# Kernel optimization log

Hardware: AMD Instinct MI355X
Metric: run time of the kernel (lower is better)

## Reference

```python
import jax, jax.numpy as jnp
import numpy as np

N = 50000      # num vertices
M = 10000      # num hyperedges
NNZ = 1600000  # incidence list length (avg degree 32)
D = 128        # in_features == out_features


def setup_inputs() -> dict:
    key = jax.random.key(0)
    k0, k1, k2, k3, k4, k5 = jax.random.split(key, 6)
    X = jax.random.normal(k0, (N, D), dtype=jnp.float32)
    X0 = jax.random.normal(k1, (N, D), dtype=jnp.float32)
    vertex = jax.random.randint(k2, (NNZ,), 0, N)
    edges = jax.random.randint(k3, (NNZ,), 0, M)
    # nn.Linear(D, D, bias=False) weight, kaiming-uniform-ish scale
    W = jax.random.uniform(k4, (D, D), dtype=jnp.float32,
                           minval=-1.0, maxval=1.0) / np.float32(np.sqrt(D))
    alpha = jax.random.uniform(k5, (), dtype=jnp.float32)
    beta = jnp.float32(0.5)
    return {"X": X, "X0": X0, "W": W, "alpha": alpha, "beta": beta,
            "vertex": vertex, "edges": edges}


def _scatter_mean(vals, idx, num_segments):
    # segment mean; empty segments -> 0 (matches torch_scatter 'mean')
    s = jax.ops.segment_sum(vals, idx, num_segments=num_segments)
    cnt = jax.ops.segment_sum(jnp.ones(idx.shape, vals.dtype), idx,
                              num_segments=num_segments)
    return s / jnp.maximum(cnt, 1.0)[:, None]


def reference(X, X0, W, alpha, beta, vertex, edges):
    Xve = X[vertex]                          # [NNZ, D] gather vertex -> incidence
    Xe = _scatter_mean(Xve, edges, M)        # [M, D]   hyperedge features
    Xev = Xe[edges]                          # [NNZ, D] gather edge -> incidence
    Xv = _scatter_mean(Xev, vertex, N)       # [N, D]   back to vertices
    Xi = (1.0 - alpha) * Xv + alpha * X0     # initial-residual mix
    return (1.0 - beta) * Xi + beta * (Xi @ W.T)  # identity-map mix + linear
```

## Files before the change

### kernel.cpp

```cpp
#include <hip/hip_runtime.h>
#include <hip/hip_bf16.h>


#define DD 128
#define NV 50000
#define ME 10000

#define CHUNK 4096
#define NEB 157
#define NVB 196
#define PB_CAP 12288

typedef __hip_bfloat16 bf16;
typedef __attribute__((ext_vector_type(8))) short short8v;
typedef __attribute__((ext_vector_type(4))) float float4v;
typedef __attribute__((ext_vector_type(4))) unsigned uint4v;

#define OFF_XE    0
#define OFF_ELIST 2560000
#define OFF_VLIST 8960000
#define OFF_EPAIR 15360000
#define OFF_VPAIR 21760000
#define OFF_XB    15360000
#define OFF_VOFF  28160000
#define OFF_EOFF  28360064
#define OFF_CBH   28400128
#define OFF_GBE   28401664
#define OFF_GBV   28402304
#define OFF_GCE   28403136
#define OFF_GCV   28403776
#define OFF_FLAG  28404608
#define OFF_WF    28404624
#define WS_USED   28470160

__device__ __forceinline__ float bf2f(unsigned short s) {
    union { unsigned u; float f; } x; x.u = ((unsigned)s) << 16; return x.f;
}
__device__ __forceinline__ unsigned f2bfu(float x) {
    union { bf16 h; unsigned short u; } c; c.h = __float2bfloat16(x); return (unsigned)c.u;
}
__device__ __forceinline__ float loadf(const void* p, long long i, unsigned f32) {
    if (f32) return ((const float*)p)[i];
    return bf2f(((const unsigned short*)p)[i]);
}
__device__ __forceinline__ float u2f_lo(unsigned x) {
    union { unsigned u; float f; } c; c.u = x << 16; return c.f;
}
__device__ __forceinline__ float u2f_hi(unsigned x) {
    union { unsigned u; float f; } c; c.u = x & 0xFFFF0000u; return c.f;
}
__device__ __forceinline__ void acc8(const uint4& u, float* a) {
    a[0] += u2f_lo(u.x); a[1] += u2f_hi(u.x);
    a[2] += u2f_lo(u.y); a[3] += u2f_hi(u.y);
    a[4] += u2f_lo(u.z); a[5] += u2f_hi(u.z);
    a[6] += u2f_lo(u.w); a[7] += u2f_hi(u.w);
}

__device__ __forceinline__ unsigned wave_is_fp32(const unsigned short* p) {
    int l = threadIdx.x & 63;
    int big = 0;
    for (int i = l; i < 256; i += 64) {
        unsigned e = (p[i] >> 7) & 0xFFu;
        if (e >= 0x90u) big++;
    }
    for (int s = 32; s > 0; s >>= 1) big += __shfl_down(big, s);
    return (__shfl(big, 0) >= 4) ? 1u : 0u;
}

__global__ __launch_bounds__(256) void prep_all(const void* X, const void* X0, const void* W,
                                                const void* beta_p,
                                                const int* __restrict__ vertex,
                                                const int* __restrict__ edges,
                                                unsigned* __restrict__ flags,
                                                unsigned short* __restrict__ Wfrag,
                                                unsigned* __restrict__ cbh, int nnz) {
    __shared__ unsigned h[NEB + NVB];
    int b = blockIdx.x, t = threadIdx.x;

    if (b == 0) {
        if (t < 64) {
            const unsigned short* px[3] = {(const unsigned short*)X,
                                           (const unsigned short*)X0,
                                           (const unsigned short*)W};
            for (int k = 0; k < 3; k++) {
                int big = 0;
                for (int i = t; i < 256; i += 64) {
                    unsigned e = (px[k][i] >> 7) & 0xFFu;
                    if (e >= 0x90u) big++;
                }
                for (int s = 32; s > 0; s >>= 1) big += __shfl_down(big, s);
                if (t == 0) flags[k] = (big >= 4) ? 1u : 0u;
            }
            if (t == 0) {
                unsigned short bb = *(const unsigned short*)beta_p;
                flags[3] = (bb == 0x3F00u) ? 0u : 1u;
            }
        }
        return;
    }

    if (b <= 8) {
        int blob = (b - 1) * 256 + t;
        unsigned fW = wave_is_fp32((const unsigned short*)W);
        unsigned short bu = *(const unsigned short*)beta_p;
        unsigned fS = (bu == 0x3F00u) ? 0u : 1u;
        int lane = blob & 63, kk = (blob >> 6) & 3, ct = blob >> 8;
        int nn = lane & 15, quad = lane >> 4;
        int c = ct * 16 + nn;
        int kbase = kk * 32 + quad * 8;
        float beta = loadf(beta_p, 0, fS);
        float omb = 1.f - beta;
        unsigned short hi[8], lo[8];
#pragma unroll
        for (int j = 0; j < 8; j++) {
            float wv = loadf(W, (long long)c * DD + kbase + j, fW);
            float v = beta * wv + ((kbase + j) == c ? omb : 0.f);
            unsigned short hh = (unsigned short)f2bfu(v);
            hi[j] = hh;
            lo[j] = (unsigned short)f2bfu(v - bf2f(hh));
        }
        uint4 ph, pl;
        ph.x = (unsigned)hi[0] | ((unsigned)hi[1] << 16);
        ph.y = (unsigned)hi[2] | ((unsigned)hi[3] << 16);
        ph.z = (unsigned)hi[4] | ((unsigned)hi[5] << 16);
        ph.w = (unsigned)hi[6] | ((unsigned)hi[7] << 16);
        pl.x = (unsigned)lo[0] | ((unsigned)lo[1] << 16);
        pl.y = (unsigned)lo[2] | ((unsigned)lo[3] << 16);
        pl.z = (unsigned)lo[4] | ((unsigned)lo[5] << 16);
        pl.w = (unsigned)lo[6] | ((unsigned)lo[7] << 16);
        ((uint4*)Wfrag)[blob] = ph;
        ((uint4*)Wfrag)[2048 + blob] = pl;
        return;
    }

    int hb = b - 9;
    for (int i = t; i < NEB + NVB; i += 256) h[i] = 0;
    __syncthreads();
    int stride = 512 * 256;
    for (int i = hb * 256 + t; i < nnz; i += stride) {
        atomicAdd(&h[edges[i] >> 6], 1u);
        atomicAdd(&h[NEB + (vertex[i] >> 8)], 1u);
    }
    __syncthreads();
    for (int i = t; i < NEB + NVB; i += 256) {
        unsigned v = h[i];
        if (v) atomicAdd(&cbh[i], v);
    }
}

__global__ __launch_bounds__(256) void conv_x(const void* __restrict__ X,
                                              unsigned short* __restrict__ Xb,
                                              const unsigned* __restrict__ flags) {
    if (!flags[0]) return;
    int i = blockIdx.x * 256 + threadIdx.x;
    if (i >= NV * DD / 8) return;
    const float4* p = (const float4*)X + (size_t)i * 2;
    float4 a = p[0], b = p[1];
    uint4 o;
    o.x = f2bfu(a.x) | (f2bfu(a.y) << 16);
    o.y = f2bfu(a.z) | (f2bfu(a.w) << 16);
    o.z = f2bfu(b.x) | (f2bfu(b.y) << 16);
    o.w = f2bfu(b.z) | (f2bfu(b.w) << 16);
    ((uint4*)Xb)[i] = o;
}

__global__ void scan353(const unsigned* __restrict__ cbh,
                        unsigned* __restrict__ gbe, unsigned* __restrict__ gbv,
                        unsigned* __restrict__ gce, unsigned* __restrict__ gcv,
                        unsigned* __restrict__ voff, unsigned* __restrict__ eoff,
                        int nnz) {
    __shared__ unsigned s[512];
    int t = threadIdx.x;
    unsigned v = (t < NEB + NVB) ? cbh[t] : 0u;
    s[t] = v;
    __syncthreads();
    for (int st = 1; st < 512; st <<= 1) {
        unsigned u = (t >= st) ? s[t - st] : 0u;
        __syncthreads();
        s[t] += u;
        __syncthreads();
    }
    unsigned excl = s[t] - v;
    if (t < NEB) {
        gbe[t] = excl; gce[t] = excl;
    } else if (t < NEB + NVB) {
        unsigned base = s[NEB - 1];
        gbv[t - NEB] = excl - base;
        gcv[t - NEB] = excl - base;
    }
    if (t == 0) {
        gbe[NEB] = (unsigned)nnz;
        gbv[NVB] = (unsigned)nnz;
        eoff[ME] = (unsigned)nnz;
        voff[NV] = (unsigned)nnz;
    }
}

__global__ __launch_bounds__(256) void build_pairs(const int* __restrict__ vertex,
                                                   const int* __restrict__ edges,
                                                   unsigned* __restrict__ gcur_e,
                                                   unsigned* __restrict__ gcur_v,
                                                   unsigned* __restrict__ epairs,
                                                   unsigned* __restrict__ vpairs, int nnz) {
    __shared__ unsigned buf[CHUNK];
    __shared__ unsigned hist[256], scn[256], loff[256], cur[256], gbase[256];
    int t = threadIdx.x;
    int base = blockIdx.x * CHUNK;
    int len = min(CHUNK, nnz - base);
    if (len <= 0) return;

    unsigned pkr[16];

    hist[t] = 0;
    __syncthreads();
#pragma unroll
    for (int it = 0; it < 16; it++) {
        int i = t + it * 256;
        if (i < len) {
            unsigned e = (unsigned)edges[base + i];
            unsigned v = (unsigned)vertex[base + i];
            unsigned pk = (e << 16) | v;
            pkr[it] = pk;
            atomicAdd(&hist[pk >> 22], 1u);
        }
    }
    __syncthreads();
    unsigned hv = hist[t];
    scn[t] = hv;
    __syncthreads();
    for (int st = 1; st < 256; st <<= 1) {
        unsigned u = (t >= st) ? scn[t - st] : 0u;
        __syncthreads();
        scn[t] += u;
        __syncthreads();
    }
    loff[t] = scn[t] - hv;
    cur[t] = scn[t] - hv;
    if (t < NEB && hv > 0) gbase[t] = atomicAdd(&gcur_e[t], hv);
    __syncthreads();
#pragma unroll
    for (int it = 0; it < 16; it++) {
        int i = t + it * 256;
        if (i < len) {
            unsigned pk = pkr[it];
            unsigned p = atomicAdd(&cur[pk >> 22], 1u);
            buf[p] = pk;
        }
    }
    __syncthreads();
    for (int i = t; i < len; i += 256) {
        unsigned pk = buf[i];
        unsigned b = pk >> 22;
        epairs[gbase[b] + (i - loff[b])] = pk;
    }

    __syncthreads();
    hist[t] = 0;
    __syncthreads();
#pragma unroll
    for (int it = 0; it < 16; it++) {
        int i = t + it * 256;
        if (i < len) {
            unsigned pk = buf[i];
            unsigned npk = (pk << 16) | (pk >> 16);
            pkr[it] = npk;
            atomicAdd(&hist[npk >> 24], 1u);
        }
    }
    __syncthreads();
    hv = hist[t];
    scn[t] = hv;
    __syncthreads();
    for (int st = 1; st < 256; st <<= 1) {
        unsigned u = (t >= st) ? scn[t - st] : 0u;
        __syncthreads();
        scn[t] += u;
        __syncthreads();
    }
    loff[t] = scn[t] - hv;
    cur[t] = scn[t] - hv;
    if (t < NVB && hv > 0) gbase[t] = atomicAdd(&gcur_v[t], hv);
    __syncthreads();
#pragma unroll
    for (int it = 0; it < 16; it++) {
        int i = t + it * 256;
        if (i < len) {
            unsigned npk = pkr[it];
            unsigned p = atomicAdd(&cur[npk >> 24], 1u);
            buf[p] = npk;
        }
    }
    __syncthreads();
    for (int i = t; i < len; i += 256) {
        unsigned npk = buf[i];
        unsigned b = npk >> 24;
        vpairs[gbase[b] + (i - loff[b])] = npk;
    }
}

__global__ __launch_bounds__(256) void build_lists(const unsigned* __restrict__ epairs,
                                                   const unsigned* __restrict__ vpairs,
                                                   const unsigned* __restrict__ gbe,
                                                   const unsigned* __restrict__ gbv,
                                                   unsigned* __restrict__ eoff,
                                                   unsigned* __restrict__ voff,
                                                   unsigned short* __restrict__ elist,
                                                   unsigned short* __restrict__ vlist) {
    __shared__ unsigned buf[PB_CAP];
    __shared__ unsigned offs[256], curs[256];
    int b = blockIdx.x, t = threadIdx.x;
    const unsigned* pairs;
    unsigned* off;
    unsigned short* list;
    unsigned s0, s1;
    int k0, nk;
    if (b < NEB) {
        pairs = epairs; off = eoff; list = elist;
        k0 = b << 6; nk = min(64, ME - k0);
        s0 = gbe[b]; s1 = gbe[b + 1];
    } else {
        int bb = b - NEB;
        pairs = vpairs; off = voff; list = vlist;
        k0 = bb << 8; nk = min(256, NV - k0);
        s0 = gbv[bb]; s1 = gbv[bb + 1];
    }
    int len = (int)(s1 - s0);

    curs[t] = 0;
    __syncthreads();
    for (int i = t; i < len; i += 256) {
        unsigned pk = pairs[s0 + i];
        atomicAdd(&curs[(pk >> 16) - k0], 1u);
    }
    __syncthreads();
    unsigned hv = curs[t];
    offs[t] = hv;
    __syncthreads();
    for (int st = 1; st < 256; st <<= 1) {
        unsigned u = (t >= st) ? offs[t - st] : 0u;
        __syncthreads();
        offs[t] += u;
        __syncthreads();
    }
    unsigned my_excl = offs[t] - hv;
    __syncthreads();
    offs[t] = my_excl;
    curs[t] = 0;
    if (t < nk) off[k0 + t] = s0 + my_excl;
    __syncthreads();

    if (len <= PB_CAP) {
        for (int i = t; i < len; i += 256) {
            unsigned pk = pairs[s0 + i];
            int lk = (int)(pk >> 16) - k0;
            unsigned p = offs[lk] + atomicAdd(&curs[lk], 1u);
            buf[p] = pk & 0xFFFFu;
        }
        __syncthreads();
        for (int i = t; i < len; i += 256) list[s0 + i] = (unsigned short)buf[i];
    } else {
        for (int i = t; i < len; i += 256) {
            unsigned pk = pairs[s0 + i];
            int lk = (int)(pk >> 16) - k0;
            unsigned p = offs[lk] + atomicAdd(&curs[lk], 1u);
            list[s0 + p] = (unsigned short)(pk & 0xFFFFu);
        }
    }
}

__global__ __launch_bounds__(256, 8) void edge_agg(const void* __restrict__ X,
                                                   const unsigned short* __restrict__ Xb,
                                                   const unsigned* __restrict__ eoff,
                                                   const unsigned short* __restrict__ elist,
                                                   unsigned short* __restrict__ Xe,
                                                   const unsigned* __restrict__ flags, int m) {
    __shared__ float red[4][DD];
    int e = blockIdx.x;
    int t = threadIdx.x, lane = t & 63, w = t >> 6;
    const unsigned short* Xp = flags[0] ? Xb : (const unsigned short*)X;
    unsigned s0 = eoff[e], s1 = eoff[e + 1];
    float a[8];
#pragma unroll
    for (int i = 0; i < 8; i++) a[i] = 0.f;

    int sub = t & 15;
    unsigned q = s0 + (unsigned)(t >> 4);
    for (; q + 48 < s1; q += 64) {
        unsigned v0 = __builtin_nontemporal_load(elist + q);
        unsigned v1 = __builtin_nontemporal_load(elist + q + 16);
        unsigned v2 = __builtin_nontemporal_load(elist + q + 32);
        unsigned v3 = __builtin_nontemporal_load(elist + q + 48);
        uint4 u0 = *(const uint4*)(Xp + (size_t)v0 * DD + 8 * sub);
        uint4 u1 = *(const uint4*)(Xp + (size_t)v1 * DD + 8 * sub);
        uint4 u2 = *(const uint4*)(Xp + (size_t)v2 * DD + 8 * sub);
        uint4 u3 = *(const uint4*)(Xp + (size_t)v3 * DD + 8 * sub);
        acc8(u0, a); acc8(u1, a); acc8(u2, a); acc8(u3, a);
    }
    for (; q + 16 < s1; q += 32) {
        unsigned v0 = __builtin_nontemporal_load(elist + q);
        unsigned v1 = __builtin_nontemporal_load(elist + q + 16);
        uint4 u0 = *(const uint4*)(Xp + (size_t)v0 * DD + 8 * sub);
        uint4 u1 = *(const uint4*)(Xp + (size_t)v1 * DD + 8 * sub);
        acc8(u0, a); acc8(u1, a);
    }
    if (q < s1) {
        unsigned v0 = __builtin_nontemporal_load(elist + q);
        uint4 u0 = *(const uint4*)(Xp + (size_t)v0 * DD + 8 * sub);
        acc8(u0, a);
    }
#pragma unroll
    for (int i = 0; i < 8; i++) {
        a[i] += __shfl_xor(a[i], 16);
        a[i] += __shfl_xor(a[i], 32);
    }
    if ((lane >> 4) == 0) {
#pragma unroll
        for (int i = 0; i < 8; i++) red[w][8 * sub + i] = a[i];
    }
    __syncthreads();
    if (t < DD) {
        float inv = (s1 > s0) ? 1.f / (float)(s1 - s0) : 1.f;
        float v = (red[0][t] + red[1][t] + red[2][t] + red[3][t]) * inv;
        Xe[(size_t)e * DD + t] = (unsigned short)f2bfu(v);
    }
}

__global__ __launch_bounds__(256, 6) void vertex_out(const unsigned short* __restrict__ Xe,
                                                     const unsigned* __restrict__ voff,
                                                     const unsigned short* __restrict__ vlist,
                                                     const void* __restrict__ X0,
                                                     const unsigned short* __restrict__ Wfrag,
                                                     const void* __restrict__ alpha_p,
                                                     void* __restrict__ out,
                                                     const unsigned* __restrict__ flags, int n) {
    __shared__ short8v A_hi[272];
    __shared__ short8v A_lo[272];
    __shared__ float x0s[2048];
    __shared__ unsigned short vidx[1024];
    __shared__ unsigned voffs[17];
    int t = threadIdx.x, lane = t & 63, w = t >> 6;
    unsigned fX = flags[0], f0 = flags[1], fS = flags[3];
    float alpha = loadf(alpha_p, 0, fS);
    float oma = 1.f - alpha;
    int v0 = blockIdx.x * 16;
    int nv = min(16, n - v0);

    if (t <= 16) voffs[t] = voff[min(v0 + t, n)];
    __syncthreads();
    unsigned sBase = voffs[0];
    int tot = (int)(voffs[16] - sBase);
    bool staged = tot <= 1024;

    if (staged) {
        for (int i = t; i < tot; i += 256)
            vidx[i] = __builtin_nontemporal_load(vlist + sBase + i);
    }
    if (!f0) {
        int cnt = nv * 16;
        const uint4v* P = (const uint4v*)((const unsigned short*)X0 + (size_t)v0 * DD);
        for (int i = t; i < cnt; i += 256) {
            uint4v u = __builtin_nontemporal_load(P + i);
            float* d = &x0s[i * 8];
            d[0] = u2f_lo(u.x); d[1] = u2f_hi(u.x);
            d[2] = u2f_lo(u.y); d[3] = u2f_hi(u.y);
            d[4] = u2f_lo(u.z); d[5] = u2f_hi(u.z);
            d[6] = u2f_lo(u.w); d[7] = u2f_hi(u.w);
        }
    } else {
        int cnt = nv * 32;
        const float4v* P = (const float4v*)((const float*)X0 + (size_t)v0 * DD);
        for (int i = t; i < cnt; i += 256) {
            float4v u = __builtin_nontemporal_load(P + i);
            *((float4v*)&x0s[i * 4]) = u;
        }
    }
    __syncthreads();

    int g = lane >> 4, sub = lane & 15;
    for (int j = 0; j < 4; j++) {
        int r = w * 4 + j, v = v0 + r;
        int idx = (sub >> 2) * 68 + (sub & 3) * 17 + r;
        float a[8];
#pragma unroll
        for (int i = 0; i < 8; i++) a[i] = 0.f;
        if (v < n) {
            unsigned ls0 = voffs[r] - sBase, ls1 = voffs[r + 1] - sBase;
            unsigned q = ls0;
            if (staged) {
                for (; q + 16 <= ls1; q += 16) {
                    unsigned e0 = vidx[q + g], e1 = vidx[q + 4 + g];
                    unsigned e2 = vidx[q + 8 + g], e3 = vidx[q + 12 + g];
                    uint4 u0 = *(const uint4*)(Xe + (size_t)e0 * DD + 8 * sub);
                    uint4 u1 = *(const uint4*)(Xe + (size_t)e1 * DD + 8 * sub);
                    uint4 u2 = *(const uint4*)(Xe + (size_t)e2 * DD + 8 * sub);
                    uint4 u3 = *(const uint4*)(Xe + (size_t)e3 * DD + 8 * sub);
                    acc8(u0, a); acc8(u1, a); acc8(u2, a); acc8(u3, a);
                }
                for (; q + 4 <= ls1; q += 4) {
                    unsigned e0 = vidx[q + g];
                    uint4 u0 = *(const uint4*)(Xe + (size_t)e0 * DD + 8 * sub);
                    acc8(u0, a);
                }
                if (g < (int)(ls1 - q)) {
                    unsigned e0 = vidx[q + g];
                    uint4 u0 = *(const uint4*)(Xe + (size_t)e0 * DD + 8 * sub);
                    acc8(u0, a);
                }
            } else {
                const unsigned short* vp = vlist + sBase;
                for (; q + 8 <= ls1; q += 8) {
                    unsigned e0 = __builtin_nontemporal_load(vp + q + g);
                    unsigned e1 = __builtin_nontemporal_load(vp + q + 4 + g);
                    uint4 u0 = *(const uint4*)(Xe + (size_t)e0 * DD + 8 * sub);
                    uint4 u1 = *(const uint4*)(Xe + (size_t)e1 * DD + 8 * sub);
                    acc8(u0, a); acc8(u1, a);
                }
                for (; q + 4 <= ls1; q += 4) {
                    unsigned e0 = __builtin_nontemporal_load(vp + q + g);
                    uint4 u0 = *(const uint4*)(Xe + (size_t)e0 * DD + 8 * sub);
                    acc8(u0, a);
                }
                if (g < (int)(ls1 - q)) {
                    unsigned e0 = __builtin_nontemporal_load(vp + q + g);
                    uint4 u0 = *(const uint4*)(Xe + (size_t)e0 * DD + 8 * sub);
                    acc8(u0, a);
                }
            }
#pragma unroll
            for (int i = 0; i < 8; i++) {
                a[i] += __shfl_xor(a[i], 16);
                a[i] += __shfl_xor(a[i], 32);
            }
            if (g == 0) {
                unsigned deg = ls1 - ls0;
                float inv = deg ? 1.f / (float)deg : 1.f;
                const float* xr = &x0s[r * 128 + 8 * sub];
                short8v ah, al;
#pragma unroll
                for (int i = 0; i < 8; i++) {
                    float xi = oma * (a[i] * inv) + alpha * xr[i];
                    unsigned short hh = (unsigned short)f2bfu(xi);
                    ah[i] = (short)hh;
                    al[i] = (short)f2bfu(xi - bf2f(hh));
                }
                A_hi[idx] = ah;
                A_lo[idx] = al;
            }
        } else if (g == 0) {
            short8v zf = {0, 0, 0, 0, 0, 0, 0, 0};
            A_hi[idx] = zf;
            A_lo[idx] = zf;
        }
    }

    __syncthreads();
    int ct = w;
    short8v ah[4], al[4];
#pragma unroll
    for (int kk = 0; kk < 4; kk++) {
        int ridx = kk * 68 + (lane >> 4) * 17 + (lane & 15);
        ah[kk] = A_hi[ridx];
        al[kk] = A_lo[ridx];
    }
    const short8v* Bh = (const short8v*)Wfrag;
    const short8v* Bl = Bh + 2048;
#pragma unroll
    for (int tt = 0; tt < 2; tt++) {
        int c2 = ct + 4 * tt;
        float4v acc = {0.f, 0.f, 0.f, 0.f};
#pragma unroll
        for (int kk = 0; kk < 4; kk++) {
            short8v bh = Bh[(c2 * 4 + kk) * 64 + lane];
            short8v bl = Bl[(c2 * 4 + kk) * 64 + lane];
            acc = __builtin_amdgcn_mfma_f32_16x16x32_bf16(ah[kk], bh, acc, 0, 0, 0);
            acc = __builtin_amdgcn_mfma_f32_16x16x32_bf16(al[kk], bh, acc, 0, 0, 0);
            acc = __builtin_amdgcn_mfma_f32_16x16x32_bf16(ah[kk], bl, acc, 0, 0, 0);
        }
        int col = c2 * 16 + (lane & 15);
        int rbase = v0 + (lane >> 4) * 4;
#pragma unroll
        for (int reg = 0; reg < 4; reg++) {
            int row = rbase + reg;
            if (row < n) {
                if (fX) {
                    __builtin_nontemporal_store(acc[reg],
                        (float*)out + (size_t)row * DD + col);
                } else {
                    bf16 hv = __float2bfloat16(acc[reg]);
                    unsigned short hb = *(unsigned short*)&hv;
                    __builtin_nontemporal_store(hb,
                        (unsigned short*)out + (size_t)row * DD + col);
                }
            }
        }
    }
}

extern "C" void kernel_launch(void* const* d_in, const int* in_sizes, int n_in,
                              void* d_out, int out_size, void* d_ws, size_t ws_size,
                              hipStream_t stream) {
    const void* X      = d_in[0];
    const void* X0     = d_in[1];
    const void* W      = d_in[2];
    const void* alpha  = d_in[3];
    const void* beta   = d_in[4];
    const int*  vertex = (const int*)d_in[5];
    const int*  edges  = (const int*)d_in[6];
    const int nnz = in_sizes[5];

    char* ws = (char*)d_ws;
    unsigned short* Xe = (unsigned short*)(ws + OFF_XE);
    unsigned short* elist = (unsigned short*)(ws + OFF_ELIST);
    unsigned short* vlist = (unsigned short*)(ws + OFF_VLIST);
    unsigned* epairs = (unsigned*)(ws + OFF_EPAIR);
    unsigned* vpairs = (unsigned*)(ws + OFF_VPAIR);
    unsigned short* Xb = (unsigned short*)(ws + OFF_XB);
    unsigned* voff   = (unsigned*)(ws + OFF_VOFF);
    unsigned* eoff   = (unsigned*)(ws + OFF_EOFF);
    unsigned* cbh    = (unsigned*)(ws + OFF_CBH);
    unsigned* gbe    = (unsigned*)(ws + OFF_GBE);
    unsigned* gbv    = (unsigned*)(ws + OFF_GBV);
    unsigned* gce    = (unsigned*)(ws + OFF_GCE);
    unsigned* gcv    = (unsigned*)(ws + OFF_GCV);
    unsigned* flags  = (unsigned*)(ws + OFF_FLAG);
    unsigned short* Wfrag = (unsigned short*)(ws + OFF_WF);

    hipMemsetAsync(ws + OFF_CBH, 0, 1536, stream);

    prep_all<<<521, 256, 0, stream>>>(X, X0, W, beta, vertex, edges,
                                      flags, Wfrag, cbh, nnz);

    scan353<<<1, 512, 0, stream>>>(cbh, gbe, gbv, gce, gcv, voff, eoff, nnz);

    int pa_blocks = (nnz + CHUNK - 1) / CHUNK;
    build_pairs<<<pa_blocks, 256, 0, stream>>>(vertex, edges, gce, gcv,
                                               epairs, vpairs, nnz);

    build_lists<<<NEB + NVB, 256, 0, stream>>>(epairs, vpairs, gbe, gbv,
                                               eoff, voff, elist, vlist);

    conv_x<<<(NV * DD / 8 + 255) / 256, 256, 0, stream>>>(X, Xb, flags);

    edge_agg<<<ME, 256, 0, stream>>>(X, Xb, eoff, elist, Xe, flags, ME);

    vertex_out<<<(NV + 15) / 16, 256, 0, stream>>>(Xe, voff, vlist, X0, Wfrag,
                                                   alpha, d_out, flags, NV);
}
```

Baseline: 255.1 us.

## Use wave-shuffle scans and fused histograms in CSR build kernels

Replaces the shared-memory Hillis-Steele scans (many __syncthreads) in scan353, build_pairs and build_lists with wave shuffle scans plus a small cross-wave combine. build_pairs now computes the edge and vertex histograms in one pass, halves CHUNK to 2048 for more blocks and fewer registers, and fuses the epairs write with the key swap. The prep histogram and build_lists loops are unrolled to batch loads, and the build_lists staging buffer shrinks to 16-bit. These aim to cut barrier and latency overhead in the preprocessing stage, at the cost of more blocks doing more global atomics on the bucket cursors.

```diff
diff --git a/kernel.cpp b/kernel.cpp
--- a/kernel.cpp
+++ b/kernel.cpp
@@ -6,7 +6,7 @@
 #define NV 50000
 #define ME 10000
 
-#define CHUNK 4096
+#define CHUNK 2048
 #define NEB 157
 #define NVB 196
 #define PB_CAP 12288
@@ -56,6 +56,15 @@
     a[6] += u2f_lo(u.w); a[7] += u2f_hi(u.w);
 }
 
+__device__ __forceinline__ unsigned wave_iscan(unsigned x, int lane) {
+#pragma unroll
+    for (int s = 1; s < 64; s <<= 1) {
+        unsigned u = __shfl_up(x, s);
+        if (lane >= s) x += u;
+    }
+    return x;
+}
+
 __device__ __forceinline__ unsigned wave_is_fp32(const unsigned short* p) {
     int l = threadIdx.x & 63;
     int big = 0;
@@ -137,14 +146,25 @@
     for (int i = t; i < NEB + NVB; i += 256) h[i] = 0;
     __syncthreads();
     int stride = 512 * 256;
-    for (int i = hb * 256 + t; i < nnz; i += stride) {
+    int i = hb * 256 + t;
+    for (; i + 3 * stride < nnz; i += 4 * stride) {
+        int e0 = edges[i],              v0 = vertex[i];
+        int e1 = edges[i + stride],     v1 = vertex[i + stride];
+        int e2 = edges[i + 2 * stride], v2 = vertex[i + 2 * stride];
+        int e3 = edges[i + 3 * stride], v3 = vertex[i + 3 * stride];
+        atomicAdd(&h[e0 >> 6], 1u); atomicAdd(&h[NEB + (v0 >> 8)], 1u);
+        atomicAdd(&h[e1 >> 6], 1u); atomicAdd(&h[NEB + (v1 >> 8)], 1u);
+        atomicAdd(&h[e2 >> 6], 1u); atomicAdd(&h[NEB + (v2 >> 8)], 1u);
+        atomicAdd(&h[e3 >> 6], 1u); atomicAdd(&h[NEB + (v3 >> 8)], 1u);
+    }
+    for (; i < nnz; i += stride) {
         atomicAdd(&h[edges[i] >> 6], 1u);
         atomicAdd(&h[NEB + (vertex[i] >> 8)], 1u);
     }
     __syncthreads();
-    for (int i = t; i < NEB + NVB; i += 256) {
-        unsigned v = h[i];
-        if (v) atomicAdd(&cbh[i], v);
+    for (int j = t; j < NEB + NVB; j += 256) {
+        unsigned v = h[j];
+        if (v) atomicAdd(&cbh[j], v);
     }
 }
 
@@ -169,24 +189,25 @@
                         unsigned* __restrict__ gce, unsigned* __restrict__ gcv,
                         unsigned* __restrict__ voff, unsigned* __restrict__ eoff,
                         int nnz) {
-    __shared__ unsigned s[512];
+    __shared__ unsigned wsum[8];
     int t = threadIdx.x;
+    int lane = t & 63, w = t >> 6;
     unsigned v = (t < NEB + NVB) ? cbh[t] : 0u;
-    s[t] = v;
-    __syncthreads();
-    for (int st = 1; st < 512; st <<= 1) {
-        unsigned u = (t >= st) ? s[t - st] : 0u;
-        __syncthreads();
-        s[t] += u;
-        __syncthreads();
-    }
-    unsigned excl = s[t] - v;
+    unsigned inc = wave_iscan(v, lane);
+    if (lane == 63) wsum[w] = inc;
+    __syncthreads();
+    if (t == 0) {
+        unsigned a = 0;
+        for (int i = 0; i < 8; i++) { unsigned x = wsum[i]; wsum[i] = a; a += x; }
+    }
+    __syncthreads();
+    inc += wsum[w];
+    unsigned excl = inc - v;
     if (t < NEB) {
         gbe[t] = excl; gce[t] = excl;
     } else if (t < NEB + NVB) {
-        unsigned base = s[NEB - 1];
-        gbv[t - NEB] = excl - base;
-        gcv[t - NEB] = excl - base;
+        gbv[t - NEB] = excl - (unsigned)nnz;
+        gcv[t - NEB] = excl - (unsigned)nnz;
     }
     if (t == 0) {
         gbe[NEB] = (unsigned)nnz;
@@ -203,91 +224,83 @@
                                                    unsigned* __restrict__ epairs,
                                                    unsigned* __restrict__ vpairs, int nnz) {
     __shared__ unsigned buf[CHUNK];
-    __shared__ unsigned hist[256], scn[256], loff[256], cur[256], gbase[256];
-    int t = threadIdx.x;
+    __shared__ unsigned hist_e[256], hist_v[256];
+    __shared__ unsigned loff[256], cur[256], gbase[256];
+    __shared__ unsigned wsum[4];
+    int t = threadIdx.x, lane = t & 63, w = t >> 6;
     int base = blockIdx.x * CHUNK;
     int len = min(CHUNK, nnz - base);
     if (len <= 0) return;
 
-    unsigned pkr[16];
-
-    hist[t] = 0;
-    __syncthreads();
-#pragma unroll
-    for (int it = 0; it < 16; it++) {
+    unsigned pkr[8];
+
+    hist_e[t] = 0; hist_v[t] = 0;
+    __syncthreads();
+#pragma unroll
+    for (int it = 0; it < 8; it++) {
         int i = t + it * 256;
         if (i < len) {
             unsigned e = (unsigned)edges[base + i];
             unsigned v = (unsigned)vertex[base + i];
             unsigned pk = (e << 16) | v;
             pkr[it] = pk;
-            atomicAdd(&hist[pk >> 22], 1u);
-        }
-    }
-    __syncthreads();
-    unsigned hv = hist[t];
-    scn[t] = hv;
-    __syncthreads();
-    for (int st = 1; st < 256; st <<= 1) {
-        unsigned u = (t >= st) ? scn[t - st] : 0u;
-        __syncthreads();
-        scn[t] += u;
-        __syncthreads();
-    }
-    loff[t] = scn[t] - hv;
-    cur[t] = scn[t] - hv;
+            atomicAdd(&hist_e[pk >> 22], 1u);
+            atomicAdd(&hist_v[(pk >> 8) & 0xFFu], 1u);
+        }
+    }
+    __syncthreads();
+
+    unsigned hv = hist_e[t];
+    unsigned inc = wave_iscan(hv, lane);
+    if (lane == 63) wsum[w] = inc;
+    __syncthreads();
+    if (t == 0) { unsigned a = 0; for (int i = 0; i < 4; i++) { unsigned x = wsum[i]; wsum[i] = a; a += x; } }
+    __syncthreads();
+    inc += wsum[w];
+    unsigned excl = inc - hv;
+    loff[t] = excl; cur[t] = excl;
     if (t < NEB && hv > 0) gbase[t] = atomicAdd(&gcur_e[t], hv);
     __syncthreads();
-#pragma unroll
-    for (int it = 0; it < 16; it++) {
+
+#pragma unroll
+    for (int it = 0; it < 8; it++) {
         int i = t + it * 256;
         if (i < len) {
             unsigned pk = pkr[it];
-            unsigned p = atomicAdd(&cur[pk >> 22], 1u);
-            buf[p] = pk;
-        }
-    }
-    __syncthreads();
-    for (int i = t; i < len; i += 256) {
-        unsigned pk = buf[i];
-        unsigned b = pk >> 22;
-        epairs[gbase[b] + (i - loff[b])] = pk;
-    }
-
-    __syncthreads();
-    hist[t] = 0;
-    __syncthreads();
-#pragma unroll
-    for (int it = 0; it < 16; it++) {
+            buf[atomicAdd(&cur[pk >> 22], 1u)] = pk;
+        }
+    }
+    __syncthreads();
+#pragma unroll
+    for (int it = 0; it < 8; it++) {
         int i = t + it * 256;
         if (i < len) {
             unsigned pk = buf[i];
-            unsigned npk = (pk << 16) | (pk >> 16);
-            pkr[it] = npk;
-            atomicAdd(&hist[npk >> 24], 1u);
-        }
-    }
-    __syncthreads();
-    hv = hist[t];
-    scn[t] = hv;
-    __syncthreads();
-    for (int st = 1; st < 256; st <<= 1) {
-        unsigned u = (t >= st) ? scn[t - st] : 0u;
-        __syncthreads();
-        scn[t] += u;
-        __syncthreads();
-    }
-    loff[t] = scn[t] - hv;
-    cur[t] = scn[t] - hv;
+            unsigned b = pk >> 22;
+            epairs[gbase[b] + (i - loff[b])] = pk;
+            pkr[it] = (pk << 16) | (pk >> 16);
+        }
+    }
+    __syncthreads();
+
+    hv = hist_v[t];
+    inc = wave_iscan(hv, lane);
+    if (lane == 63) wsum[w] = inc;
+    __syncthreads();
+    if (t == 0) { unsigned a = 0; for (int i = 0; i < 4; i++) { unsigned x = wsum[i]; wsum[i] = a; a += x; } }
+    __syncthreads();
+    inc += wsum[w];
+    excl = inc - hv;
+    loff[t] = excl; cur[t] = excl;
     if (t < NVB && hv > 0) gbase[t] = atomicAdd(&gcur_v[t], hv);
     __syncthreads();
-#pragma unroll
-    for (int it = 0; it < 16; it++) {
+
+#pragma unroll
+    for (int it = 0; it < 8; it++) {
         int i = t + it * 256;
         if (i < len) {
             unsigned npk = pkr[it];
-            unsigned p = atomicAdd(&cur[npk >> 24], 1u);
-            buf[p] = npk;
+            buf[atomicAdd(&cur[npk >> 24], 1u)] = npk;
         }
     }
     __syncthreads();
@@ -306,9 +319,11 @@
                                                    unsigned* __restrict__ voff,
                                                    unsigned short* __restrict__ elist,
                                                    unsigned short* __restrict__ vlist) {
-    __shared__ unsigned buf[PB_CAP];
+    __shared__ unsigned short buf[PB_CAP];
     __shared__ unsigned offs[256], curs[256];
+    __shared__ unsigned wsum[4];
     int b = blockIdx.x, t = threadIdx.x;
+    int lane = t & 63, w = t >> 6;
     const unsigned* pairs;
     unsigned* off;
     unsigned short* list;
@@ -328,36 +343,54 @@
 
     curs[t] = 0;
     __syncthreads();
-    for (int i = t; i < len; i += 256) {
-        unsigned pk = pairs[s0 + i];
-        atomicAdd(&curs[(pk >> 16) - k0], 1u);
+    for (int i0 = 0; i0 < len; i0 += 2048) {
+        unsigned pks[8];
+#pragma unroll
+        for (int it = 0; it < 8; it++) {
+            int i = i0 + t + it * 256;
+            if (i < len) pks[it] = pairs[s0 + i];
+        }
+#pragma unroll
+        for (int it = 0; it < 8; it++) {
+            int i = i0 + t + it * 256;
+            if (i < len) atomicAdd(&curs[(pks[it] >> 16) - k0], 1u);
+        }
     }
     __syncthreads();
     unsigned hv = curs[t];
-    offs[t] = hv;
-    __syncthreads();
-    for (int st = 1; st < 256; st <<= 1) {
-        unsigned u = (t >= st) ? offs[t - st] : 0u;
-        __syncthreads();
-        offs[t] += u;
-        __syncthreads();
-    }
-    unsigned my_excl = offs[t] - hv;
-    __syncthreads();
+    unsigned inc = wave_iscan(hv, lane);
+    if (lane == 63) wsum[w] = inc;
+    __syncthreads();
+    if (t == 0) { unsigned a = 0; for (int i = 0; i < 4; i++) { unsigned x = wsum[i]; wsum[i] = a; a += x; } }
+    __syncthreads();
+    inc += wsum[w];
+    unsigned my_excl = inc - hv;
     offs[t] = my_excl;
     curs[t] = 0;
     if (t < nk) off[k0 + t] = s0 + my_excl;
     __syncthreads();
 
     if (len <= PB_CAP) {
-        for (int i = t; i < len; i += 256) {
-            unsigned pk = pairs[s0 + i];
-            int lk = (int)(pk >> 16) - k0;
-            unsigned p = offs[lk] + atomicAdd(&curs[lk], 1u);
-            buf[p] = pk & 0xFFFFu;
+        for (int i0 = 0; i0 < len; i0 += 2048) {
+            unsigned pks[8];
+#pragma unroll
+            for (int it = 0; it < 8; it++) {
+                int i = i0 + t + it * 256;
+                if (i < len) pks[it] = pairs[s0 + i];
+            }
+#pragma unroll
+            for (int it = 0; it < 8; it++) {
+                int i = i0 + t + it * 256;
+                if (i < len) {
+                    unsigned pk = pks[it];
+                    int lk = (int)(pk >> 16) - k0;
+                    unsigned p = offs[lk] + atomicAdd(&curs[lk], 1u);
+                    buf[p] = (unsigned short)(pk & 0xFFFFu);
+                }
+            }
         }
         __syncthreads();
-        for (int i = t; i < len; i += 256) list[s0 + i] = (unsigned short)buf[i];
+        for (int i = t; i < len; i += 256) list[s0 + i] = buf[i];
     } else {
         for (int i = t; i < len; i += 256) {
             unsigned pk = pairs[s0 + i];
```

Result: no change. 251.4 us (-1.4%).
